# Performance work log

Measured on AMD Instinct MI355X. Metric: run time of the kernel, lower is better.

## Reference

```python
import jax, jax.numpy as jnp
import numpy as np
from jax import lax

PS = 64          # patch_size
K = 256          # num_train_patches
COARSE = 4       # down_size_rate
TEMP = 0.1


def _avg_pool_stride(x, k):
    # avg_pool2d(x, kernel=k, stride=k); x: [B,1,H,W], H,W divisible by k
    B, C, H, W = x.shape
    return x.reshape(B, C, H // k, k, W // k, k).mean(axis=(3, 5))


def _avg_pool_s1(x, k):
    # avg_pool2d(x, kernel=k, stride=1, padding=VALID)
    s = lax.reduce_window(x, 0.0, lax.add, (1, 1, k, k), (1, 1, 1, 1), 'VALID')
    return s / float(k * k)


def _resize_bilinear(x, oh, ow):
    # F.interpolate mode='bilinear', align_corners=False; x: [B,1,H,W]
    B, C, H, W = x.shape

    def coords(n_in, n_out):
        c = (jnp.arange(n_out, dtype=jnp.float32) + 0.5) * (n_in / n_out) - 0.5
        c = jnp.clip(c, 0.0, n_in - 1)
        c0 = jnp.floor(c).astype(jnp.int32)
        c1 = jnp.minimum(c0 + 1, n_in - 1)
        return c0, c1, c - c0

    y0, y1, wy = coords(H, oh)
    x0, x1, wx = coords(W, ow)
    v00 = x[:, :, y0[:, None], x0[None, :]]
    v01 = x[:, :, y0[:, None], x1[None, :]]
    v10 = x[:, :, y1[:, None], x0[None, :]]
    v11 = x[:, :, y1[:, None], x1[None, :]]
    wy = wy[:, None]
    top = v00 * (1 - wx) + v01 * wx
    bot = v10 * (1 - wx) + v11 * wx
    return top * (1 - wy) + bot * wy


def _select_starts(coarse_pred, H, W, key):
    # coarse_pred: [B,1,H/COARSE,W/COARSE] -> sampled (h_starts, w_starts) [B,K]
    stride = max(1, PS // 8)
    coarse_kernel = max(1, PS // COARSE)
    fg = coarse_pred[:, 0:1]
    coarse_scores = _avg_pool_s1(fg, coarse_kernel)
    grid_h = (H - PS) // stride + 1
    grid_w = (W - PS) // stride + 1
    scores_map = _resize_bilinear(coarse_scores, grid_h, grid_w)
    flat = scores_map.reshape(scores_map.shape[0], -1)  # [B, grid_h*grid_w]
    smin = flat.min(axis=1, keepdims=True)
    smax = flat.max(axis=1, keepdims=True)
    rng = jnp.maximum(smax - smin, 1e-6)
    scaled = (flat - smin) / rng / TEMP  # logits of softmax probs
    # multinomial-without-replacement == Gumbel top-k on logits
    g = jax.random.gumbel(key, scaled.shape, dtype=scaled.dtype)
    _, top_idx = lax.top_k(scaled + g, K)  # [B,K]
    rows = top_idx // grid_w
    cols = top_idx % grid_w
    return rows * stride, cols * stride


def _gather_patches(img, h_starts, w_starts):
    # img: [B,C,H,W]; starts: [B,K] -> [B,K,C,PS,PS]
    C = img.shape[1]

    def one(im, h, w):  # im [C,H,W]
        return lax.dynamic_slice(im, (0, h, w), (C, PS, PS))

    return jax.vmap(jax.vmap(one, in_axes=(None, 0, 0)), in_axes=(0, 0, 0))(
        img, h_starts, w_starts)


def setup_inputs() -> dict:
    key = jax.random.key(0)
    k1, k2 = jax.random.split(key)
    image = jax.random.normal(k1, (8, 3, 1024, 1024), dtype=jnp.float32)
    labels = jax.random.uniform(k2, (8, 1, 1024, 1024), dtype=jnp.float32)
    return {"image": image, "labels": labels}


def reference(image, labels):
    B, C, H, W = image.shape
    coarse_pred = _avg_pool_stride(labels, COARSE)       # global branch (oracle)
    key = jax.random.key(42)
    h_starts, w_starts = _select_starts(coarse_pred, H, W, key)
    patches = _gather_patches(image, h_starts, w_starts)         # [B,K,C,PS,PS]
    label_patches = _gather_patches(labels, h_starts, w_starts)  # [B,K,1,PS,PS]
    coords = jnp.stack([h_starts, w_starts], axis=-1)            # [B,K,2]
    return patches, label_patches, coords
```

## Files before the change

kernel.cpp:

```cpp
#include <hip/hip_runtime.h>
#include <hip/hip_bf16.h>
#include <stdint.h>

#define B_     8
#define CSW    241
#define CSG    61
#define GW     121
#define NPB    14641
#define KSEL   256
#define TOTG   117128

#define NSEG   16
#define SEGLEN 916

#define PATCH_OFF   0
#define LABEL_OFF   25165824
#define COORD_OFF   33554432

#define FG_OFF    0
#define CS_OFF    524288
#define FLAT_OFF  988936
#define MM_OFF    1106064
#define CAND_OFF  1340336

__device__ __forceinline__ unsigned enc_f(float f) {
  unsigned s = __float_as_uint(f);
  return (s & 0x80000000u) ? ~s : (s | 0x80000000u);
}
__device__ __forceinline__ float dec_f(unsigned o) {
  unsigned s = (o & 0x80000000u) ? (o & 0x7FFFFFFFu) : ~o;
  return __uint_as_float(s);
}

__global__ void k_fg(const float* __restrict__ labels, float* __restrict__ fg) {
  int idx = blockIdx.x * 256 + threadIdx.x;
  int b = idx >> 16; int rem = idx & 65535;
  int oy = rem >> 8; int ox = rem & 255;
  const float4* p = (const float4*)(labels + (size_t)b * 1048576 +
                                    (size_t)oy * 4096 + ox * 4);
  float acc = 0.0f;
  #pragma unroll
  for (int dy = 0; dy < 4; ++dy) {
    float4 v = p[dy * 256];
    acc = __fadd_rn(acc, v.x); acc = __fadd_rn(acc, v.y);
    acc = __fadd_rn(acc, v.z); acc = __fadd_rn(acc, v.w);
  }
  fg[idx] = __fdiv_rn(acc, 16.0f);
}

__global__ void k_cs(const float* __restrict__ fg, float* __restrict__ cs,
                     unsigned* __restrict__ mm) {
  if (blockIdx.x == 0 && threadIdx.x < 16)
    mm[threadIdx.x] = (threadIdx.x < 8) ? 0xFFFFFFFFu : 0u;

  int idx = blockIdx.x * 256 + threadIdx.x;
  const int TOT = B_ * CSW * CSG;
  if (idx >= TOT) return;
  int b = idx / (CSW * CSG); int rem = idx % (CSW * CSG);
  int oy = rem / CSG; int ox0 = (rem % CSG) * 4;
  int nk = min(4, CSW - ox0);
  int lv = nk + 15;
  const float* p = fg + (size_t)b * 65536 + (size_t)oy * 256 + ox0;

  float acc[4] = {0.0f, 0.0f, 0.0f, 0.0f};
  for (int wy = 0; wy < 16; ++wy) {
    const float* r = p + wy * 256;
    float v[19];
    #pragma unroll
    for (int x = 0; x < 19; ++x) { v[x] = 0.0f; if (x < lv) v[x] = r[x]; }
    #pragma unroll
    for (int k = 0; k < 4; ++k) {
      if (k < nk) {
        #pragma unroll
        for (int wx = 0; wx < 16; ++wx) acc[k] = __fadd_rn(acc[k], v[k + wx]);
      }
    }
  }
  float* co = cs + (size_t)b * (CSW * CSW) + (size_t)oy * CSW + ox0;
  #pragma unroll
  for (int k = 0; k < 4; ++k)
    if (k < nk) co[k] = __fdiv_rn(acc[k], 256.0f);
}

__global__ void k_resize(const float* __restrict__ cs, float* __restrict__ flat,
                         unsigned* __restrict__ mm) {
  __shared__ unsigned smn[256], smx[256];
  int b = blockIdx.y;
  int rem = blockIdx.x * 256 + threadIdx.x;
  int tid = threadIdx.x;
  unsigned mn = 0xFFFFFFFFu, mx = 0u;

  if (rem < NPB) {
    int oy = rem / GW; int ox = rem % GW;
    const float SCALE = (float)(241.0 / 121.0);

    float cy = __fsub_rn(__fmul_rn(__fadd_rn((float)oy, 0.5f), SCALE), 0.5f);
    cy = fminf(fmaxf(cy, 0.0f), 240.0f);
    int y0 = (int)floorf(cy); int y1 = min(y0 + 1, 240);
    float wy = __fsub_rn(cy, (float)y0);

    float cx = __fsub_rn(__fmul_rn(__fadd_rn((float)ox, 0.5f), SCALE), 0.5f);
    cx = fminf(fmaxf(cx, 0.0f), 240.0f);
    int x0 = (int)floorf(cx); int x1 = min(x0 + 1, 240);
    float wx = __fsub_rn(cx, (float)x0);

    const float* base = cs + (size_t)b * (CSW * CSW);
    float v00 = base[y0 * CSW + x0];
    float v01 = base[y0 * CSW + x1];
    float v10 = base[y1 * CSW + x0];
    float v11 = base[y1 * CSW + x1];
    float omwx = __fsub_rn(1.0f, wx), omwy = __fsub_rn(1.0f, wy);
    float top = __fadd_rn(__fmul_rn(v00, omwx), __fmul_rn(v01, wx));
    float bot = __fadd_rn(__fmul_rn(v10, omwx), __fmul_rn(v11, wx));
    float val = __fadd_rn(__fmul_rn(top, omwy), __fmul_rn(bot, wy));
    flat[(size_t)b * NPB + rem] = val;
    unsigned o = enc_f(val);
    mn = o; mx = o;
  }
  smn[tid] = mn; smx[tid] = mx; __syncthreads();
  for (int s = 128; s > 0; s >>= 1) {
    if (tid < s) {
      smn[tid] = min(smn[tid], smn[tid + s]);
      smx[tid] = max(smx[tid], smx[tid + s]);
    }
    __syncthreads();
  }
  if (tid == 0) {
    atomicMin(&mm[b], smn[0]);
    atomicMax(&mm[8 + b], smx[0]);
  }
}

__device__ __forceinline__ void tf2(unsigned c0, unsigned c1,
                                    unsigned* o0, unsigned* o1) {
  const unsigned ks0 = 0u, ks1 = 42u, ks2 = 0x1BD11BDAu ^ 0u ^ 42u;
  unsigned x0 = c0 + ks0, x1 = c1 + ks1;
#define RND(r) { x0 += x1; x1 = (x1 << r) | (x1 >> (32 - r)); x1 ^= x0; }
  RND(13) RND(15) RND(26) RND(6)   x0 += ks1; x1 += ks2 + 1u;
  RND(17) RND(29) RND(16) RND(24)  x0 += ks2; x1 += ks0 + 2u;
  RND(13) RND(15) RND(26) RND(6)   x0 += ks0; x1 += ks1 + 3u;
  RND(17) RND(29) RND(16) RND(24)  x0 += ks1; x1 += ks2 + 4u;
  RND(13) RND(15) RND(26) RND(6)   x0 += ks2; x1 += ks0 + 5u;
#undef RND
  *o0 = x0; *o1 = x1;
}

__global__ void k_part(const float* __restrict__ flat, const unsigned* __restrict__ mm,
                       unsigned long long* __restrict__ cand) {
  __shared__ unsigned long long sm[1024];
  int blk = blockIdx.x;
  int b = blk >> 4, s = blk & 15;
  int base = s * SEGLEN;
  int len = min(SEGLEN, NPB - base);
  int tid = threadIdx.x;

  float smin = dec_f(mm[b]), smax = dec_f(mm[8 + b]);
  float rng = fmaxf(__fsub_rn(smax, smin), 1e-6f);

  for (int i = tid; i < 1024; i += 256) {
    unsigned long long kv = 0ull;
    if (i < len) {
      int j = base + i;
      int idx = b * NPB + j;
      float scaled = __fdiv_rn(__fdiv_rn(__fsub_rn(flat[idx], smin), rng), 0.1f);

      unsigned o0, o1;
      tf2(0u, (unsigned)idx, &o0, &o1);
      unsigned bits = o0 ^ o1;

      unsigned m = bits >> 9;
      float u = (m == 0u) ? 1.17549435e-38f
                          : __fsub_rn(__uint_as_float(0x3f800000u | m), 1.0f);
      float l1 = (float)::log((double)u);
      float a  = -l1;
      float l2 = (float)::log((double)a);
      float g  = -l2;

      float tot = __fadd_rn(scaled, g);
      unsigned o = enc_f(tot);
      kv = ((unsigned long long)o << 32) | (unsigned long long)((unsigned)j ^ 0xFFFFFFFFu);
    }
    sm[i] = kv;
  }
  __syncthreads();

  for (int ksz = 2; ksz <= 1024; ksz <<= 1) {
    for (int j = ksz >> 1; j > 0; j >>= 1) {
      for (int i = tid; i < 1024; i += 256) {
        int ixj = i ^ j;
        if (ixj > i) {
          bool up = ((i & ksz) == 0);
          unsigned long long a = sm[i], c = sm[ixj];
          if ((a > c) == up) { sm[i] = c; sm[ixj] = a; }
        }
      }
      __syncthreads();
    }
  }
  cand[(size_t)blk * 256 + tid] = sm[1023 - tid];
}

__global__ void k_merge(const unsigned long long* __restrict__ cand,
                        float* __restrict__ coords) {
  __shared__ unsigned long long sm[4096];
  int b = blockIdx.x, tid = threadIdx.x;
  const unsigned long long* cb = cand + (size_t)b * 4096;
  for (int t = tid; t < 4096; t += 256) sm[t] = cb[t];
  __syncthreads();

  int g = 1;
  for (int m = NSEG; m > 1; m >>= 1, g <<= 1) {
    int half = m >> 1;
    for (int q = tid; q < half * 256; q += 256) {
      int p = q >> 8, i = q & 255;
      int A = (2 * p) * g * 256, Bb = (2 * p + 1) * g * 256;
      unsigned long long a = sm[A + i], c = sm[Bb + 255 - i];
      sm[A + i] = a > c ? a : c;
    }
    __syncthreads();
    for (int j = 128; j > 0; j >>= 1) {
      for (int q = tid; q < half * 128; q += 256) {
        int p = q >> 7, r = q & 127;
        int i = ((r & ~(j - 1)) << 1) | (r & (j - 1));
        int A = (2 * p) * g * 256;
        unsigned long long a = sm[A + i], c = sm[A + i + j];
        if (a < c) { sm[A + i] = c; sm[A + i + j] = a; }
      }
      __syncthreads();
    }
  }

  unsigned long long key = sm[tid];
  unsigned j = ((unsigned)(key & 0xFFFFFFFFull)) ^ 0xFFFFFFFFu;
  int row = j / GW, col = j % GW;
  coords[((size_t)b * KSEL + tid) * 2 + 0] = (float)(row * 8);
  coords[((size_t)b * KSEL + tid) * 2 + 1] = (float)(col * 8);
}

__global__ void k_gather(const float* __restrict__ image, const float* __restrict__ labels,
                         float* __restrict__ out) {
  int bk = blockIdx.x;
  int b = bk >> 8;
  const float* coords = out + COORD_OFF;
  int h = (int)coords[(size_t)bk * 2 + 0];
  int w = (int)coords[(size_t)bk * 2 + 1];

  const float* imgb = image + (size_t)b * 3145728;
  float4* po = (float4*)(out + PATCH_OFF + (size_t)bk * 12288);
  for (int t = threadIdx.x; t < 3072; t += 256) {
    int c = t >> 10, rem = t & 1023, y = rem >> 4, x4 = rem & 15;
    po[t] = *(const float4*)(imgb + (size_t)c * 1048576 +
                             (size_t)(h + y) * 1024 + w + x4 * 4);
  }
  const float* labb = labels + (size_t)b * 1048576;
  float4* lo = (float4*)(out + LABEL_OFF + (size_t)bk * 4096);
  for (int t = threadIdx.x; t < 1024; t += 256) {
    int y = t >> 4, x4 = t & 15;
    lo[t] = *(const float4*)(labb + (size_t)(h + y) * 1024 + w + x4 * 4);
  }
}

extern "C" void kernel_launch(void* const* d_in, const int* in_sizes, int n_in,
                              void* d_out, int out_size, void* d_ws, size_t ws_size,
                              hipStream_t stream) {
  const float* image  = (const float*)d_in[0];
  const float* labels = (const float*)d_in[1];
  float* out = (float*)d_out;

  float* fg   = out + FG_OFF;
  float* cs   = out + CS_OFF;
  float* flat = out + FLAT_OFF;
  unsigned* mm = (unsigned*)(out + MM_OFF);
  unsigned long long* cand = (unsigned long long*)(out + CAND_OFF);
  float* coords = out + COORD_OFF;

  k_fg<<<2048, 256, 0, stream>>>(labels, fg);
  k_cs<<<(B_ * CSW * CSG + 255) / 256, 256, 0, stream>>>(fg, cs, mm);
  k_resize<<<dim3((NPB + 255) / 256, B_), 256, 0, stream>>>(cs, flat, mm);
  k_part<<<B_ * NSEG, 256, 0, stream>>>(flat, mm, cand);
  k_merge<<<B_, 256, 0, stream>>>(cand, coords);
  k_gather<<<2048, 256, 0, stream>>>(image, labels, out);
}
```

Before: 309.9 us.

## Register/shuffle bitonic sort in partition and merge, nontemporal gather stores

```diff
diff --git a/kernel.cpp b/kernel.cpp
--- a/kernel.cpp
+++ b/kernel.cpp
@@ -22,6 +22,8 @@
 #define FLAT_OFF  988936
 #define MM_OFF    1106064
 #define CAND_OFF  1340336
+
+typedef float floatx4 __attribute__((ext_vector_type(4)));
 
 __device__ __forceinline__ unsigned enc_f(float f) {
   unsigned s = __float_as_uint(f);
@@ -157,7 +159,10 @@
   float smin = dec_f(mm[b]), smax = dec_f(mm[8 + b]);
   float rng = fmaxf(__fsub_rn(smax, smin), 1e-6f);
 
-  for (int i = tid; i < 1024; i += 256) {
+  unsigned long long e[4];
+  #pragma unroll
+  for (int q = 0; q < 4; ++q) {
+    int i = q * 256 + tid;
     unsigned long long kv = 0ull;
     if (i < len) {
       int j = base + i;
@@ -180,54 +185,109 @@
       unsigned o = enc_f(tot);
       kv = ((unsigned long long)o << 32) | (unsigned long long)((unsigned)j ^ 0xFFFFFFFFu);
     }
-    sm[i] = kv;
-  }
-  __syncthreads();
+    e[q] = kv;
+  }
 
   for (int ksz = 2; ksz <= 1024; ksz <<= 1) {
     for (int j = ksz >> 1; j > 0; j >>= 1) {
-      for (int i = tid; i < 1024; i += 256) {
-        int ixj = i ^ j;
-        if (ixj > i) {
+      if (j >= 256) {
+        int dq = j >> 8;
+        #pragma unroll
+        for (int q = 0; q < 4; ++q) {
+          if ((q & dq) == 0) {
+            int q2 = q | dq;
+            int i0 = q * 256 + tid;
+            bool up = ((i0 & ksz) == 0);
+            unsigned long long a = e[q], c = e[q2];
+            unsigned long long mn = a < c ? a : c, mx = a < c ? c : a;
+            e[q]  = up ? mn : mx;
+            e[q2] = up ? mx : mn;
+          }
+        }
+      } else if (j >= 64) {
+        #pragma unroll
+        for (int q = 0; q < 4; ++q) sm[q * 256 + tid] = e[q];
+        __syncthreads();
+        #pragma unroll
+        for (int q = 0; q < 4; ++q) {
+          int i = q * 256 + tid;
+          unsigned long long a = e[q], c = sm[i ^ j];
           bool up = ((i & ksz) == 0);
-          unsigned long long a = sm[i], c = sm[ixj];
-          if ((a > c) == up) { sm[i] = c; sm[ixj] = a; }
+          bool lowside = ((i & j) == 0);
+          bool take_min = (lowside == up);
+          unsigned long long mn = a < c ? a : c, mx = a < c ? c : a;
+          e[q] = take_min ? mn : mx;
         }
-      }
-      __syncthreads();
-    }
-  }
-  cand[(size_t)blk * 256 + tid] = sm[1023 - tid];
+        __syncthreads();
+      } else {
+        #pragma unroll
+        for (int q = 0; q < 4; ++q) {
+          int i = q * 256 + tid;
+          unsigned long long a = e[q];
+          unsigned long long c = __shfl_xor(a, j, 64);
+          bool up = ((i & ksz) == 0);
+          bool lowside = ((i & j) == 0);
+          bool take_min = (lowside == up);
+          unsigned long long mn = a < c ? a : c, mx = a < c ? c : a;
+          e[q] = take_min ? mn : mx;
+        }
+      }
+    }
+  }
+  cand[(size_t)blk * 256 + (255 - tid)] = e[3];
 }
 
 __global__ void k_merge(const unsigned long long* __restrict__ cand,
                         float* __restrict__ coords) {
   __shared__ unsigned long long sm[4096];
   int b = blockIdx.x, tid = threadIdx.x;
-  const unsigned long long* cb = cand + (size_t)b * 4096;
-  for (int t = tid; t < 4096; t += 256) sm[t] = cb[t];
+  int w = tid >> 6, l = tid & 63;
+  const ulonglong2* cb2 = (const ulonglong2*)(cand + (size_t)b * 4096);
+  for (int t = tid; t < 2048; t += 256) {
+    ulonglong2 v = cb2[t];
+    sm[2 * t] = v.x; sm[2 * t + 1] = v.y;
+  }
   __syncthreads();
 
   int g = 1;
   for (int m = NSEG; m > 1; m >>= 1, g <<= 1) {
     int half = m >> 1;
-    for (int q = tid; q < half * 256; q += 256) {
-      int p = q >> 8, i = q & 255;
+    for (int p = w; p < half; p += 4) {
       int A = (2 * p) * g * 256, Bb = (2 * p + 1) * g * 256;
-      unsigned long long a = sm[A + i], c = sm[Bb + 255 - i];
-      sm[A + i] = a > c ? a : c;
+      unsigned long long r[4];
+      #pragma unroll
+      for (int eIdx = 0; eIdx < 4; ++eIdx) {
+        int i = eIdx * 64 + l;
+        unsigned long long a = sm[A + i], c = sm[Bb + 255 - i];
+        r[eIdx] = a > c ? a : c;
+      }
+      {
+        unsigned long long a0 = r[0], a2 = r[2];
+        r[0] = a0 > a2 ? a0 : a2; r[2] = a0 > a2 ? a2 : a0;
+        unsigned long long a1 = r[1], a3 = r[3];
+        r[1] = a1 > a3 ? a1 : a3; r[3] = a1 > a3 ? a3 : a1;
+      }
+      {
+        unsigned long long a0 = r[0], a1 = r[1];
+        r[0] = a0 > a1 ? a0 : a1; r[1] = a0 > a1 ? a1 : a0;
+        unsigned long long a2 = r[2], a3 = r[3];
+        r[2] = a2 > a3 ? a2 : a3; r[3] = a2 > a3 ? a3 : a2;
+      }
+      #pragma unroll
+      for (int j = 32; j > 0; j >>= 1) {
+        #pragma unroll
+        for (int eIdx = 0; eIdx < 4; ++eIdx) {
+          unsigned long long a = r[eIdx];
+          unsigned long long c = __shfl_xor(a, j, 64);
+          bool low = ((l & j) == 0);
+          unsigned long long mx = a > c ? a : c, mn = a > c ? c : a;
+          r[eIdx] = low ? mx : mn;
+        }
+      }
+      #pragma unroll
+      for (int eIdx = 0; eIdx < 4; ++eIdx) sm[A + eIdx * 64 + l] = r[eIdx];
     }
     __syncthreads();
-    for (int j = 128; j > 0; j >>= 1) {
-      for (int q = tid; q < half * 128; q += 256) {
-        int p = q >> 7, r = q & 127;
-        int i = ((r & ~(j - 1)) << 1) | (r & (j - 1));
-        int A = (2 * p) * g * 256;
-        unsigned long long a = sm[A + i], c = sm[A + i + j];
-        if (a < c) { sm[A + i] = c; sm[A + i + j] = a; }
-      }
-      __syncthreads();
-    }
   }
 
   unsigned long long key = sm[tid];
@@ -246,17 +306,19 @@
   int w = (int)coords[(size_t)bk * 2 + 1];
 
   const float* imgb = image + (size_t)b * 3145728;
-  float4* po = (float4*)(out + PATCH_OFF + (size_t)bk * 12288);
+  floatx4* po = (floatx4*)(out + PATCH_OFF + (size_t)bk * 12288);
   for (int t = threadIdx.x; t < 3072; t += 256) {
     int c = t >> 10, rem = t & 1023, y = rem >> 4, x4 = rem & 15;
-    po[t] = *(const float4*)(imgb + (size_t)c * 1048576 +
-                             (size_t)(h + y) * 1024 + w + x4 * 4);
+    floatx4 v = *(const floatx4*)(imgb + (size_t)c * 1048576 +
+                                  (size_t)(h + y) * 1024 + w + x4 * 4);
+    __builtin_nontemporal_store(v, &po[t]);
   }
   const float* labb = labels + (size_t)b * 1048576;
-  float4* lo = (float4*)(out + LABEL_OFF + (size_t)bk * 4096);
+  floatx4* lo = (floatx4*)(out + LABEL_OFF + (size_t)bk * 4096);
   for (int t = threadIdx.x; t < 1024; t += 256) {
     int y = t >> 4, x4 = t & 15;
-    lo[t] = *(const float4*)(labb + (size_t)(h + y) * 1024 + w + x4 * 4);
+    floatx4 v = *(const floatx4*)(labb + (size_t)(h + y) * 1024 + w + x4 * 4);
+    __builtin_nontemporal_store(v, &lo[t]);
   }
 }
 
```

New measurement: 293.8 us. -5.2%, faster.
